# Performance work log

Measured on AMD Instinct MI355X. Metric: run time of the kernel, lower is better.

## Reference

```python
import jax, jax.numpy as jnp
import numpy as np

EPS = 1e-5


def _gcn_norm(edge_index, N):
    # symmetric GCN normalization with self-loops: D^-1/2 (A+I) D^-1/2
    row, col = edge_index[0], edge_index[1]
    loop = jnp.arange(N, dtype=row.dtype)
    row_f = jnp.concatenate([row, loop])
    col_f = jnp.concatenate([col, loop])
    deg = jax.ops.segment_sum(jnp.ones_like(row_f, dtype=jnp.float32), row_f, num_segments=N)
    dinv = jnp.where(deg > 0, jax.lax.rsqrt(jnp.maximum(deg, 1.0)), 0.0)
    norm = dinv[row_f] * dinv[col_f]  # [E+N]
    return row_f, col_f, norm


def _gcn_conv(h, W, b, row_f, col_f, norm, N):
    h = h @ W  # [N, C_out] small GEMM
    msg = h[col_f] * norm[:, None]  # gather over edges  [E+N, C_out]
    return jax.ops.segment_sum(msg, row_f, num_segments=N) + b


def _bn_eval(h, gamma, beta, mean, var):
    return (h - mean) * jax.lax.rsqrt(var + EPS) * gamma + beta


def setup_inputs() -> dict:
    key = jax.random.key(0)
    ks = jax.random.split(key, 12)
    N, E = 100000, 1600000
    C_in, C_hid, C_out = 64, 64, 64
    x = jax.random.normal(ks[0], (N, C_in), dtype=jnp.float32)
    edge_index = jax.random.randint(ks[1], (2, E), 0, N, dtype=jnp.int32)
    s = 1.0 / np.sqrt(C_hid)
    inp = {
        "x": x,
        "edge_index": edge_index,
        "W1": jax.random.normal(ks[2], (C_in, C_hid), dtype=jnp.float32) * s,
        "b1": jnp.zeros((C_hid,), jnp.float32),
        "g1": jnp.ones((C_hid,), jnp.float32),
        "be1": jnp.zeros((C_hid,), jnp.float32),
        "m1": jax.random.normal(ks[3], (C_hid,), dtype=jnp.float32) * 0.1,
        "v1": jax.random.uniform(ks[4], (C_hid,), minval=0.5, maxval=1.5, dtype=jnp.float32),
        "W2": jax.random.normal(ks[5], (C_hid, C_hid), dtype=jnp.float32) * s,
        "b2": jnp.zeros((C_hid,), jnp.float32),
        "g2": jnp.ones((C_hid,), jnp.float32),
        "be2": jnp.zeros((C_hid,), jnp.float32),
        "m2": jax.random.normal(ks[6], (C_hid,), dtype=jnp.float32) * 0.1,
        "v2": jax.random.uniform(ks[7], (C_hid,), minval=0.5, maxval=1.5, dtype=jnp.float32),
        "W3": jax.random.normal(ks[8], (C_hid, C_out), dtype=jnp.float32) * s,
        "b3": jnp.zeros((C_out,), jnp.float32),
    }
    return inp


def reference(x, edge_index, W1, b1, g1, be1, m1, v1, W2, b2, g2, be2, m2, v2, W3, b3):
    N = x.shape[0]
    row_f, col_f, norm = _gcn_norm(edge_index, N)  # cached=True: computed once
    h = _gcn_conv(x, W1, b1, row_f, col_f, norm, N)
    h = jax.nn.relu(_bn_eval(h, g1, be1, m1, v1))  # dropout off (eval)
    h = _gcn_conv(h, W2, b2, row_f, col_f, norm, N)
    h = jax.nn.relu(_bn_eval(h, g2, be2, m2, v2))
    global_embeddings = h
    hc_predictions = _gcn_conv(global_embeddings, W3, b3, row_f, col_f, norm, N)
    return (global_embeddings, hc_predictions)
```

## Files before the change

### kernel.cpp

```cpp
#include <hip/hip_runtime.h>

typedef __attribute__((ext_vector_type(8))) short bfrag8;
typedef __attribute__((ext_vector_type(4))) float facc4;
typedef __attribute__((ext_vector_type(8))) unsigned short u16x8;

#define CROWS  256
#define NCBMAX 512
#define CAP    8192
#define CHUNK  4096
#define SLACK  772
#define BPITCH (CAP + SLACK)

static __device__ __forceinline__ float bf2f(ushort u) {
    union { unsigned int i; float f; } x;
    x.i = ((unsigned int)u) << 16;
    return x.f;
}
static __device__ __forceinline__ ushort f2bf(float f) {
    union { float f; unsigned int i; } x;
    x.f = f;
    unsigned int r = x.i + 0x7FFFu + ((x.i >> 16) & 1u);
    return (ushort)(r >> 16);
}

__global__ void k_prep(const float* __restrict__ W1, const float* __restrict__ W2,
                       const float* __restrict__ W3,
                       const float* __restrict__ b1, const float* __restrict__ g1,
                       const float* __restrict__ be1, const float* __restrict__ m1,
                       const float* __restrict__ v1,
                       const float* __restrict__ b2, const float* __restrict__ g2,
                       const float* __restrict__ be2, const float* __restrict__ m2,
                       const float* __restrict__ v2,
                       const float* __restrict__ b3,
                       ushort* __restrict__ wp, float* __restrict__ pp) {
    int l = blockIdx.x;
    const float* W = (l == 0) ? W1 : (l == 1) ? W2 : W3;
    ushort* wo = wp + l * 4096;
    for (int idx = threadIdx.x; idx < 4096; idx += blockDim.x) {
        int j = idx & 7, m = (idx >> 3) & 15, quad = (idx >> 7) & 3;
        int ks = (idx >> 9) & 1, c2 = idx >> 10;
        wo[idx] = f2bf(W[(32 * ks + 8 * quad + j) * 64 + c2 * 16 + m]);
    }
    if (threadIdx.x < 64) {
        int ch = threadIdx.x;
        float PS, PH;
        if (l == 0) {
            float sc = g1[ch] * rsqrtf(v1[ch] + 1e-5f);
            PS = sc; PH = be1[ch] - m1[ch] * sc + b1[ch] * sc;
        } else if (l == 1) {
            float sc = g2[ch] * rsqrtf(v2[ch] + 1e-5f);
            PS = sc; PH = be2[ch] - m2[ch] * sc + b2[ch] * sc;
        } else {
            PS = 1.f; PH = b3[ch];
        }
        pp[l * 128 + ch] = PS;
        pp[l * 128 + 64 + ch] = PH;
    }
}


__global__ void k_cinit(int* __restrict__ ccur, int ncb,
                        ushort* __restrict__ ta, ushort* __restrict__ tb, int N) {
    int b = blockIdx.x * blockDim.x + threadIdx.x;
    if (b < ncb) ccur[b] = b * CAP;
    if (blockIdx.x == 0 && threadIdx.x < 64) {
        ta[(size_t)N * 64 + threadIdx.x] = 0;
        tb[(size_t)N * 64 + threadIdx.x] = 0;
    }
}

__global__ void k_part(const int* __restrict__ row, const int* __restrict__ col, int E,
                       int* __restrict__ ccur, int* __restrict__ bkt, int ncb) {
    __shared__ int recs[CHUNK];
    __shared__ unsigned short cbl[CHUNK];
    __shared__ int hist[NCBMAX], lbase[NCBMAX], loff[NCBMAX];
    int tid = threadIdx.x;
    int chunk0 = blockIdx.x * CHUNK;
    for (int i = tid; i < ncb; i += blockDim.x) hist[i] = 0;
    __syncthreads();
    for (int j = tid; j < CHUNK; j += blockDim.x) {
        int e = chunk0 + j;
        if (e < E) {
            int r = row[e];
            int cb = r >> 8;
            recs[j] = ((r & (CROWS - 1)) << 17) | col[e];
            cbl[j] = (unsigned short)cb;
            atomicAdd(&hist[cb], 1);
        } else cbl[j] = 0xFFFF;
    }
    __syncthreads();
    for (int i = tid; i < ncb; i += blockDim.x) {
        int h = hist[i];
        lbase[i] = h ? atomicAdd(&ccur[i], h) : 0;
        loff[i] = 0;
    }
    __syncthreads();
    for (int j = tid; j < CHUNK; j += blockDim.x) {
        unsigned short cb = cbl[j];
        if (cb != 0xFFFF) {
            int p = lbase[cb] + atomicAdd(&loff[cb], 1);
            if (p < (cb + 1) * CAP) bkt[p] = recs[j];
        }
    }
}

__global__ void k_build(const int* __restrict__ bkt, const int* __restrict__ ccur,
                        int* __restrict__ rptr, int* __restrict__ deg,
                        float* __restrict__ dinv, int* __restrict__ cidx, int N) {
    __shared__ int hist[CROWS], wstart[CROWS], cur[CROWS], psum[CROWS];
    int tid = threadIdx.x;
    int b = blockIdx.x;
    int lo = b * CROWS;
    int nr = min(CROWS, N - lo);
    int in0 = b * CAP;
    int cntE = min(ccur[b] - in0, CAP);
    int out0 = b * BPITCH;

    if (tid < CROWS) hist[tid] = 0;
    __syncthreads();
    for (int i = tid; i < cntE; i += blockDim.x)
        atomicAdd(&hist[bkt[in0 + i] >> 17], 1);
    __syncthreads();
    int d = 0, ep = 0;
    if (tid < CROWS) {
        d = hist[tid];
        ep = (d + 3) & ~3;
        psum[tid] = ep;
    }
    __syncthreads();
    #pragma unroll
    for (int off = 1; off < CROWS; off <<= 1) {
        int t = (tid >= off && tid < CROWS) ? psum[tid - off] : 0;
        __syncthreads();
        if (tid < CROWS) psum[tid] += t;
        __syncthreads();
    }
    if (tid < CROWS) {
        int ws = out0 + psum[tid] - ep;
        wstart[tid] = ws;
        cur[tid] = ws;
        if (tid < nr) {
            rptr[lo + tid] = ws;
            deg[lo + tid] = d;
            dinv[lo + tid] = rsqrtf((float)(d + 1));
        }
    }
    __syncthreads();
    for (int i = tid; i < cntE; i += blockDim.x) {
        int v = bkt[in0 + i];
        int p = atomicAdd(&cur[v >> 17], 1);
        cidx[p] = v & 0x1FFFF;
    }
    __syncthreads();
    if (tid < nr) {
        int dd = hist[tid];
        int epp = (dd + 3) & ~3;
        for (int j = dd; j < epp; j++) cidx[wstart[tid] + j] = N;
    }
}

__global__ void k_gemm(const float* __restrict__ Hv, const ushort* __restrict__ wq,
                       const float* __restrict__ dinv,
                       ushort* __restrict__ T, int ntiles, int N) {
    int lane = threadIdx.x & 63;
    int wid = (blockIdx.x * blockDim.x + threadIdx.x) >> 6;
    int nw = (gridDim.x * blockDim.x) >> 6;
    int m = lane & 15, quad = lane >> 4;

    bfrag8 bf[2][4];
    #pragma unroll
    for (int s = 0; s < 2; s++)
        #pragma unroll
        for (int c = 0; c < 4; c++)
            bf[s][c] = *(const bfrag8*)(wq +
                (size_t)((((c * 2 + s) * 4 + quad) * 16 + m) * 8));

    for (int t = wid; t < ntiles; t += nw) {
        int nodeA = t * 16 + m;
        if (nodeA >= N) nodeA = N - 1;
        bfrag8 a0, a1;
        const float* arow = Hv + (size_t)nodeA * 64;
        #pragma unroll
        for (int s = 0; s < 2; s++) {
            float4 u0 = *(const float4*)(arow + s * 32 + quad * 8);
            float4 u1 = *(const float4*)(arow + s * 32 + quad * 8 + 4);
            bfrag8 f;
            f[0] = (short)f2bf(u0.x); f[1] = (short)f2bf(u0.y);
            f[2] = (short)f2bf(u0.z); f[3] = (short)f2bf(u0.w);
            f[4] = (short)f2bf(u1.x); f[5] = (short)f2bf(u1.y);
            f[6] = (short)f2bf(u1.z); f[7] = (short)f2bf(u1.w);
            if (s == 0) a0 = f; else a1 = f;
        }
        facc4 acc[4];
        #pragma unroll
        for (int c = 0; c < 4; c++) { acc[c][0]=0.f; acc[c][1]=0.f; acc[c][2]=0.f; acc[c][3]=0.f; }
        #pragma unroll
        for (int c = 0; c < 4; c++) {
            acc[c] = __builtin_amdgcn_mfma_f32_16x16x32_bf16(a0, bf[0][c], acc[c], 0, 0, 0);
            acc[c] = __builtin_amdgcn_mfma_f32_16x16x32_bf16(a1, bf[1][c], acc[c], 0, 0, 0);
        }
        #pragma unroll
        for (int c = 0; c < 4; c++)
            #pragma unroll
            for (int r = 0; r < 4; r++) {
                int node = t * 16 + quad * 4 + r;
                if (node < N)
                    T[(size_t)node * 64 + c * 16 + m] = f2bf(dinv[node] * acc[c][r]);
            }
    }
}

template <bool FUSE>
__global__ void __launch_bounds__(256, 6)
k_aggf(const ushort* __restrict__ T2, const int* __restrict__ rptr,
       const int* __restrict__ deg, const float* __restrict__ dinv,
       const int* __restrict__ cidx,
       const float* __restrict__ pp, int relu,
       const ushort* __restrict__ wq,
       float* __restrict__ outf, ushort* __restrict__ Tn, int N) {
    __shared__ ushort lds_h[32][72];

    int tid = threadIdx.x;
    int lane = tid & 63;
    int wl = tid >> 6;
    int grp = lane >> 3;
    int s = lane & 7;
    int loc = wl * 8 + grp;
    int r = blockIdx.x * 32 + loc;
    bool rv = (r < N);
    int rs = rv ? r : N;

    int start = rv ? rptr[r] : 0;
    int ep = rv ? ((deg[r] + 3) & ~3) : 0;
    u16x8 sf = *(const u16x8*)(T2 + (size_t)rs * 64 + s * 8);
    float dr = rv ? dinv[r] : 0.f;

    float a[8];
    #pragma unroll
    for (int k = 0; k < 8; k++) a[k] = 0.f;

    int i = 0;
    bool have8 = (8 <= ep);
    int4 c4, d4;
    if (have8) {
        c4 = *(const int4*)(cidx + start);
        d4 = *(const int4*)(cidx + start + 4);
    }
    while (have8) {
        int ni = i + 8;
        bool nhave = (ni + 8 <= ep);
        int4 nc4, nd4;
        if (nhave) {
            nc4 = *(const int4*)(cidx + start + ni);
            nd4 = *(const int4*)(cidx + start + ni + 4);
        }
        u16x8 t0 = *(const u16x8*)(T2 + (size_t)c4.x * 64 + s * 8);
        u16x8 t1 = *(const u16x8*)(T2 + (size_t)c4.y * 64 + s * 8);
        u16x8 t2 = *(const u16x8*)(T2 + (size_t)c4.z * 64 + s * 8);
        u16x8 t3 = *(const u16x8*)(T2 + (size_t)c4.w * 64 + s * 8);
        u16x8 t4 = *(const u16x8*)(T2 + (size_t)d4.x * 64 + s * 8);
        u16x8 t5 = *(const u16x8*)(T2 + (size_t)d4.y * 64 + s * 8);
        u16x8 t6 = *(const u16x8*)(T2 + (size_t)d4.z * 64 + s * 8);
        u16x8 t7 = *(const u16x8*)(T2 + (size_t)d4.w * 64 + s * 8);
        #pragma unroll
        for (int k = 0; k < 8; k++)
            a[k] += ((bf2f(t0[k]) + bf2f(t1[k])) + (bf2f(t2[k]) + bf2f(t3[k]))) +
                    ((bf2f(t4[k]) + bf2f(t5[k])) + (bf2f(t6[k]) + bf2f(t7[k])));
        c4 = nc4; d4 = nd4; i = ni; have8 = nhave;
    }
    if (i < ep) {
        int4 e4 = *(const int4*)(cidx + start + i);
        u16x8 t0 = *(const u16x8*)(T2 + (size_t)e4.x * 64 + s * 8);
        u16x8 t1 = *(const u16x8*)(T2 + (size_t)e4.y * 64 + s * 8);
        u16x8 t2 = *(const u16x8*)(T2 + (size_t)e4.z * 64 + s * 8);
        u16x8 t3 = *(const u16x8*)(T2 + (size_t)e4.w * 64 + s * 8);
        #pragma unroll
        for (int k = 0; k < 8; k++)
            a[k] += (bf2f(t0[k]) + bf2f(t1[k])) + (bf2f(t2[k]) + bf2f(t3[k]));
    }

    float4 ps0 = *(const float4*)(pp + s * 8);
    float4 ps1 = *(const float4*)(pp + s * 8 + 4);
    float4 ph0 = *(const float4*)(pp + 64 + s * 8);
    float4 ph1 = *(const float4*)(pp + 64 + s * 8 + 4);
    float PS[8] = {ps0.x, ps0.y, ps0.z, ps0.w, ps1.x, ps1.y, ps1.z, ps1.w};
    float PH[8] = {ph0.x, ph0.y, ph0.z, ph0.w, ph1.x, ph1.y, ph1.z, ph1.w};

    float v[8];
    #pragma unroll
    for (int k = 0; k < 8; k++) v[k] = 0.f;
    if (rv) {
        #pragma unroll
        for (int k = 0; k < 8; k++) {
            v[k] = dr * (a[k] + bf2f(sf[k])) * PS[k] + PH[k];
            if (relu) v[k] = fmaxf(v[k], 0.f);
        }
        if (outf) {
            *(float4*)(outf + (size_t)r * 64 + s * 8) = make_float4(v[0], v[1], v[2], v[3]);
            *(float4*)(outf + (size_t)r * 64 + s * 8 + 4) = make_float4(v[4], v[5], v[6], v[7]);
        }
    }

    if constexpr (FUSE) {
        u16x8 hv;
        #pragma unroll
        for (int k = 0; k < 8; k++) hv[k] = rv ? f2bf(v[k]) : (ushort)0;
        *(u16x8*)&lds_h[loc][s * 8] = hv;

        int m = lane & 15, quad = lane >> 4;
        int rtile = wl >> 1, chalf = wl & 1;
        bfrag8 bw[2][2];
        #pragma unroll
        for (int ks = 0; ks < 2; ks++)
            #pragma unroll
            for (int c = 0; c < 2; c++)
                bw[ks][c] = *(const bfrag8*)(wq +
                    (size_t)(((((chalf * 2 + c) * 2 + ks) * 4 + quad) * 16 + m) * 8));
        __syncthreads();

        bfrag8 a0 = *(const bfrag8*)&lds_h[rtile * 16 + m][quad * 8];
        bfrag8 a1 = *(const bfrag8*)&lds_h[rtile * 16 + m][32 + quad * 8];
        facc4 acc[2];
        #pragma unroll
        for (int c = 0; c < 2; c++) { acc[c][0]=0.f; acc[c][1]=0.f; acc[c][2]=0.f; acc[c][3]=0.f; }
        #pragma unroll
        for (int c = 0; c < 2; c++) {
            acc[c] = __builtin_amdgcn_mfma_f32_16x16x32_bf16(a0, bw[0][c], acc[c], 0, 0, 0);
            acc[c] = __builtin_amdgcn_mfma_f32_16x16x32_bf16(a1, bw[1][c], acc[c], 0, 0, 0);
        }
        int nodeBase = blockIdx.x * 32 + rtile * 16;
        #pragma unroll
        for (int c = 0; c < 2; c++)
            #pragma unroll
            for (int rr = 0; rr < 4; rr++) {
                int node = nodeBase + quad * 4 + rr;
                if (node < N)
                    Tn[(size_t)node * 64 + (chalf * 2 + c) * 16 + m] =
                        f2bf(dinv[node] * acc[c][rr]);
            }
    }
}


extern "C" void kernel_launch(void* const* d_in, const int* in_sizes, int n_in,
                              void* d_out, int out_size, void* d_ws, size_t ws_size,
                              hipStream_t stream) {
    const float* x  = (const float*)d_in[0];
    const int*   ei = (const int*)d_in[1];
    const float *W1 = (const float*)d_in[2],  *b1 = (const float*)d_in[3];
    const float *g1 = (const float*)d_in[4],  *be1= (const float*)d_in[5];
    const float *m1 = (const float*)d_in[6],  *v1 = (const float*)d_in[7];
    const float *W2 = (const float*)d_in[8],  *b2 = (const float*)d_in[9];
    const float *g2 = (const float*)d_in[10], *be2= (const float*)d_in[11];
    const float *m2 = (const float*)d_in[12], *v2 = (const float*)d_in[13];
    const float *W3 = (const float*)d_in[14], *b3 = (const float*)d_in[15];

    int N = in_sizes[0] / 64;
    int E = in_sizes[1] / 2;
    const int* row = ei;
    const int* col = ei + E;
    int ncb = (N + CROWS - 1) / CROWS;

    char* p = (char*)d_ws;
    auto take = [&](size_t b) -> char* {
        char* q = p;
        p += (b + 255) & ~(size_t)255;
        return q;
    };
    int*    ccur  = (int*)   take((size_t)ncb * 4);
    int*    rptr  = (int*)   take((size_t)N * 4);
    int*    deg   = (int*)   take((size_t)N * 4);
    float*  dinv  = (float*) take((size_t)N * 4);
    ushort* wp    = (ushort*)take((size_t)3 * 4096 * 2);
    float*  pp    = (float*) take((size_t)3 * 128 * 4);
    int*    bkt   = (int*)   take((size_t)ncb * CAP * 4);
    int*    cidx  = (int*)   take((size_t)ncb * BPITCH * 4 + 1024);
    ushort* ta    = (ushort*)take((size_t)(N + 1) * 64 * 2);
    ushort* tb    = (ushort*)take((size_t)(N + 1) * 64 * 2);

    const int TB = 256;
    const int TBP = 1024;
    int nchunks = (E + CHUNK - 1) / CHUNK;
    k_prep <<<3, TB, 0, stream>>>(W1, W2, W3, b1, g1, be1, m1, v1,
                                  b2, g2, be2, m2, v2, b3, wp, pp);
    k_cinit<<<(ncb + TB - 1) / TB, TB, 0, stream>>>(ccur, ncb, ta, tb, N);
    k_part <<<nchunks, TBP, 0, stream>>>(row, col, E, ccur, bkt, ncb);
    k_build<<<ncb, TBP, 0, stream>>>(bkt, ccur, rptr, deg, dinv, cidx, N);

    float* outp = (float*)d_out;
    int ntiles = (N + 15) >> 4;
    int GG = (ntiles + 3) / 4;
    int GA = (N + 31) / 32;

    k_gemm<<<GG, TB, 0, stream>>>(x, wp, dinv, ta, ntiles, N);
    k_aggf<true><<<GA, TB, 0, stream>>>(ta, rptr, deg, dinv, cidx, pp, 1,
                                        wp + 4096, (float*)nullptr, tb, N);
    k_aggf<true><<<GA, TB, 0, stream>>>(tb, rptr, deg, dinv, cidx, pp + 128, 1,
                                        wp + 8192, outp, ta, N);
    k_aggf<false><<<GA, TB, 0, stream>>>(ta, rptr, deg, dinv, cidx, pp + 256, 0,
                                         (const ushort*)nullptr,
                                         outp + (size_t)N * 64, (ushort*)nullptr, N);
}
```

Measured before the change: 258.9 us.

## Merge init into prep kernel, shrink partition chunks, sort rows by degree

Merges the cursor and pad-row initialisation into the weight-prep kernel as a fourth block, which removes one launch. The partition chunk is halved and the partition and build kernels now run 512-thread blocks, to raise occupancy and reduce contention on the shared-memory atomics. The aggregation kernel now ranks its 32 rows by degree inside each block, so that rows of similar degree share a wavefront and lane-group imbalance drops. This adds a small ranking step with two extra barriers per block, and makes more blocks do global atomics on the bucket cursors.

```diff
diff --git a/kernel.cpp b/kernel.cpp
--- a/kernel.cpp
+++ b/kernel.cpp
@@ -7,7 +7,7 @@
 #define CROWS  256
 #define NCBMAX 512
 #define CAP    8192
-#define CHUNK  4096
+#define CHUNK  2048
 #define SLACK  772
 #define BPITCH (CAP + SLACK)
 
@@ -32,45 +32,46 @@
                        const float* __restrict__ be2, const float* __restrict__ m2,
                        const float* __restrict__ v2,
                        const float* __restrict__ b3,
-                       ushort* __restrict__ wp, float* __restrict__ pp) {
+                       ushort* __restrict__ wp, float* __restrict__ pp,
+                       int* __restrict__ ccur, int ncb,
+                       ushort* __restrict__ ta, ushort* __restrict__ tb, int N) {
     int l = blockIdx.x;
-    const float* W = (l == 0) ? W1 : (l == 1) ? W2 : W3;
-    ushort* wo = wp + l * 4096;
-    for (int idx = threadIdx.x; idx < 4096; idx += blockDim.x) {
-        int j = idx & 7, m = (idx >> 3) & 15, quad = (idx >> 7) & 3;
-        int ks = (idx >> 9) & 1, c2 = idx >> 10;
-        wo[idx] = f2bf(W[(32 * ks + 8 * quad + j) * 64 + c2 * 16 + m]);
-    }
-    if (threadIdx.x < 64) {
-        int ch = threadIdx.x;
-        float PS, PH;
-        if (l == 0) {
-            float sc = g1[ch] * rsqrtf(v1[ch] + 1e-5f);
-            PS = sc; PH = be1[ch] - m1[ch] * sc + b1[ch] * sc;
-        } else if (l == 1) {
-            float sc = g2[ch] * rsqrtf(v2[ch] + 1e-5f);
-            PS = sc; PH = be2[ch] - m2[ch] * sc + b2[ch] * sc;
-        } else {
-            PS = 1.f; PH = b3[ch];
-        }
-        pp[l * 128 + ch] = PS;
-        pp[l * 128 + 64 + ch] = PH;
-    }
-}
-
-
-__global__ void k_cinit(int* __restrict__ ccur, int ncb,
-                        ushort* __restrict__ ta, ushort* __restrict__ tb, int N) {
-    int b = blockIdx.x * blockDim.x + threadIdx.x;
-    if (b < ncb) ccur[b] = b * CAP;
-    if (blockIdx.x == 0 && threadIdx.x < 64) {
-        ta[(size_t)N * 64 + threadIdx.x] = 0;
-        tb[(size_t)N * 64 + threadIdx.x] = 0;
-    }
-}
-
-__global__ void k_part(const int* __restrict__ row, const int* __restrict__ col, int E,
-                       int* __restrict__ ccur, int* __restrict__ bkt, int ncb) {
+    if (l < 3) {
+        const float* W = (l == 0) ? W1 : (l == 1) ? W2 : W3;
+        ushort* wo = wp + l * 4096;
+        for (int idx = threadIdx.x; idx < 4096; idx += blockDim.x) {
+            int j = idx & 7, m = (idx >> 3) & 15, quad = (idx >> 7) & 3;
+            int ks = (idx >> 9) & 1, c2 = idx >> 10;
+            wo[idx] = f2bf(W[(32 * ks + 8 * quad + j) * 64 + c2 * 16 + m]);
+        }
+        if (threadIdx.x < 64) {
+            int ch = threadIdx.x;
+            float PS, PH;
+            if (l == 0) {
+                float sc = g1[ch] * rsqrtf(v1[ch] + 1e-5f);
+                PS = sc; PH = be1[ch] - m1[ch] * sc + b1[ch] * sc;
+            } else if (l == 1) {
+                float sc = g2[ch] * rsqrtf(v2[ch] + 1e-5f);
+                PS = sc; PH = be2[ch] - m2[ch] * sc + b2[ch] * sc;
+            } else {
+                PS = 1.f; PH = b3[ch];
+            }
+            pp[l * 128 + ch] = PS;
+            pp[l * 128 + 64 + ch] = PH;
+        }
+    } else {
+        for (int b = threadIdx.x; b < ncb; b += blockDim.x) ccur[b] = b * CAP;
+        if (threadIdx.x < 128) {
+            int t = threadIdx.x;
+            if (t < 64) ta[(size_t)N * 64 + t] = 0;
+            else        tb[(size_t)N * 64 + (t - 64)] = 0;
+        }
+    }
+}
+
+__global__ void __launch_bounds__(512)
+k_part(const int* __restrict__ row, const int* __restrict__ col, int E,
+       int* __restrict__ ccur, int* __restrict__ bkt, int ncb) {
     __shared__ int recs[CHUNK];
     __shared__ unsigned short cbl[CHUNK];
     __shared__ int hist[NCBMAX], lbase[NCBMAX], loff[NCBMAX];
@@ -104,9 +105,10 @@
     }
 }
 
-__global__ void k_build(const int* __restrict__ bkt, const int* __restrict__ ccur,
-                        int* __restrict__ rptr, int* __restrict__ deg,
-                        float* __restrict__ dinv, int* __restrict__ cidx, int N) {
+__global__ void __launch_bounds__(512)
+k_build(const int* __restrict__ bkt, const int* __restrict__ ccur,
+        int* __restrict__ rptr, int* __restrict__ deg,
+        float* __restrict__ dinv, int* __restrict__ cidx, int N) {
     __shared__ int hist[CROWS], wstart[CROWS], cur[CROWS], psum[CROWS];
     int tid = threadIdx.x;
     int b = blockIdx.x;
@@ -219,19 +221,39 @@
        const ushort* __restrict__ wq,
        float* __restrict__ outf, ushort* __restrict__ Tn, int N) {
     __shared__ ushort lds_h[32][72];
+    __shared__ int sdeg[32], sord[32];
 
     int tid = threadIdx.x;
     int lane = tid & 63;
     int wl = tid >> 6;
     int grp = lane >> 3;
     int s = lane & 7;
-    int loc = wl * 8 + grp;
+
+    if (tid < 32) {
+        int rr = blockIdx.x * 32 + tid;
+        sdeg[tid] = (rr < N) ? deg[rr] : -1;
+    }
+    __syncthreads();
+    if (tid < 32) {
+        int dd = sdeg[tid];
+        int rank = 0;
+        #pragma unroll
+        for (int j = 0; j < 32; j++) {
+            int dj = sdeg[j];
+            rank += (dj < dd) || (dj == dd && j < tid);
+        }
+        sord[rank] = tid;
+    }
+    __syncthreads();
+
+    int loc = sord[wl * 8 + grp];
     int r = blockIdx.x * 32 + loc;
-    bool rv = (r < N);
+    int d = sdeg[loc];
+    bool rv = (d >= 0);
     int rs = rv ? r : N;
 
     int start = rv ? rptr[r] : 0;
-    int ep = rv ? ((deg[r] + 3) & ~3) : 0;
+    int ep = rv ? ((d + 3) & ~3) : 0;
     u16x8 sf = *(const u16x8*)(T2 + (size_t)rs * 64 + s * 8);
     float dr = rv ? dinv[r] : 0.f;
 
@@ -379,13 +401,12 @@
     ushort* tb    = (ushort*)take((size_t)(N + 1) * 64 * 2);
 
     const int TB = 256;
-    const int TBP = 1024;
     int nchunks = (E + CHUNK - 1) / CHUNK;
-    k_prep <<<3, TB, 0, stream>>>(W1, W2, W3, b1, g1, be1, m1, v1,
-                                  b2, g2, be2, m2, v2, b3, wp, pp);
-    k_cinit<<<(ncb + TB - 1) / TB, TB, 0, stream>>>(ccur, ncb, ta, tb, N);
-    k_part <<<nchunks, TBP, 0, stream>>>(row, col, E, ccur, bkt, ncb);
-    k_build<<<ncb, TBP, 0, stream>>>(bkt, ccur, rptr, deg, dinv, cidx, N);
+    k_prep <<<4, TB, 0, stream>>>(W1, W2, W3, b1, g1, be1, m1, v1,
+                                  b2, g2, be2, m2, v2, b3, wp, pp,
+                                  ccur, ncb, ta, tb, N);
+    k_part <<<nchunks, 512, 0, stream>>>(row, col, E, ccur, bkt, ncb);
+    k_build<<<ncb, 512, 0, stream>>>(bkt, ccur, rptr, deg, dinv, cidx, N);
 
     float* outp = (float*)d_out;
     int ntiles = (N + 15) >> 4;
```

Result: slower. 271.7 us (+4.9%).
